# Kernel optimization log

Hardware: AMD Instinct MI355X
Metric: run time of the kernel (lower is better)

Reference implementation:

```python
import jax, jax.numpy as jnp
import numpy as np

D_MODEL = 256; N_HEADS = 8; D_FF = 1024; N_LAYERS = 8; N_BLOCKS = 4
VOCAB = 10000; N_SPARSE = 26; N_DENSE = 13; BATCH = 4096
SEQ = N_DENSE + N_SPARSE  # 39 feature tokens


def _ln(x, g, b, eps=1e-5):
    m = jnp.mean(x, -1, keepdims=True)
    v = jnp.mean((x - m) ** 2, -1, keepdims=True)
    return (x - m) * jax.lax.rsqrt(v + eps) * g + b


def _normalize(x, axis=-1, eps=1e-12):
    n = jnp.maximum(jnp.linalg.norm(x, axis=axis, keepdims=True), eps)
    return x / n


def setup_inputs() -> dict:
    key = jax.random.key(0)
    ks = iter(jax.random.split(key, 64))
    d, L, ff = D_MODEL, N_LAYERS, D_FF
    w = lambda shape: jax.random.normal(next(ks), shape, dtype=jnp.float32) * 0.02
    z = lambda shape: jnp.zeros(shape, jnp.float32)
    o = lambda shape: jnp.ones(shape, jnp.float32)
    return {
        "dense_x": jax.random.normal(next(ks), (BATCH, N_DENSE), dtype=jnp.float32),
        "sparse_x": jax.random.randint(next(ks), (BATCH, N_SPARSE), 0, VOCAB, dtype=jnp.int32),
        "W_dense": w((N_DENSE * d, N_DENSE)), "b_dense": z((N_DENSE * d,)),
        "emb": w((N_SPARSE, VOCAB + 1, d)),
        "Wq": w((L, d, d)), "bq": z((L, d)),
        "Wk": w((L, d, d)), "bk": z((L, d)),
        "Wv": w((L, d, d)), "bv": z((L, d)),
        "W1": w((L, ff, d)), "b1": z((L, ff)),
        "W2": w((L, d, ff)), "b2": z((L, d)),
        "n1g": o((L, d)), "n1b": z((L, d)),
        "n2g": o((L, d)), "n2b": z((L, d)),
        "qvec": w((N_BLOCKS, d)),
        "mha_in_w": w((3 * d, d)), "mha_in_b": z((3 * d,)),
        "mha_out_w": w((d, d)), "mha_out_b": z((d,)),
        "ng": o((d,)), "ngb": z((d,)),
        "Wo1": w((D_FF, SEQ * d)), "bo1": z((D_FF,)),
        "Wo2": w((1, D_FF)), "bo2": z((1,)),
    }


def reference(dense_x, sparse_x, W_dense, b_dense, emb, Wq, bq, Wk, bk, Wv, bv,
              W1, b1, W2, b2, n1g, n1b, n2g, n2b, qvec,
              mha_in_w, mha_in_b, mha_out_w, mha_out_b, ng, ngb,
              Wo1, bo1, Wo2, bo2):
    B = dense_x.shape[0]; d = D_MODEL; H = N_HEADS; dh = d // H
    # --- embed_features ---
    dense_emb = (dense_x @ W_dense.T + b_dense).reshape(B, N_DENSE, d)
    emb0 = emb.at[:, 0, :].set(0.0)  # padding_idx=0
    sp = emb0[jnp.arange(N_SPARSE), sparse_x]  # [B, 26, d]
    x = jnp.concatenate([dense_emb, sp], axis=1)  # [B, 39, d]

    scale = 1.0 / jnp.sqrt(jnp.float32(d))  # note: d_model, not head_dim
    block_size = N_LAYERS // N_BLOCKS
    block_outputs = [x]
    for i in range(N_LAYERS):
        # --- HSTU layer: sigmoid pointwise attention ---
        r = x
        h = _ln(x, n1g[i], n1b[i])
        q = (h @ Wq[i].T + bq[i]).reshape(B, SEQ, H, dh).transpose(0, 2, 1, 3)
        k = (h @ Wk[i].T + bk[i]).reshape(B, SEQ, H, dh).transpose(0, 2, 1, 3)
        v = (h @ Wv[i].T + bv[i]).reshape(B, SEQ, H, dh).transpose(0, 2, 1, 3)
        aw = jax.nn.sigmoid(jnp.einsum('bhqd,bhkd->bhqk', q, k) * scale)
        ao = jnp.einsum('bhqk,bhkd->bhqd', aw, v).transpose(0, 2, 1, 3).reshape(B, SEQ, d)
        x = r + ao
        r = x
        h = _ln(x, n2g[i], n2b[i])
        x = r + (jax.nn.relu(h @ W1[i].T + b1[i]) @ W2[i].T + b2[i])
        # --- AttentionResidual block mixing ---
        if (i + 1) % block_size == 0 and i < N_LAYERS - 1:
            V = jnp.stack(block_outputs + [x])  # [n, B, T, d]
            K = _normalize(V)
            qi = min(len(block_outputs), N_BLOCKS - 1)
            qn = _normalize(qvec[qi], axis=0)
            logits = jnp.einsum('d,nbtd->nbt', qn, K)
            wt = jax.nn.softmax(logits, axis=0)
            x = jnp.einsum('nbt,nbtd->btd', wt, V)
            block_outputs.append(x)

    # --- final LayerNorm + standard MHA residual ---
    r = x
    h = _ln(x, ng, ngb)
    qkv = h @ mha_in_w.T + mha_in_b
    q, k, v = jnp.split(qkv, 3, axis=-1)
    q = q.reshape(B, SEQ, H, dh).transpose(0, 2, 1, 3)
    k = k.reshape(B, SEQ, H, dh).transpose(0, 2, 1, 3)
    v = v.reshape(B, SEQ, H, dh).transpose(0, 2, 1, 3)
    at = jax.nn.softmax(jnp.einsum('bhqd,bhkd->bhqk', q, k) / jnp.sqrt(jnp.float32(dh)), axis=-1)
    mo = jnp.einsum('bhqk,bhkd->bhqd', at, v).transpose(0, 2, 1, 3).reshape(B, SEQ, d)
    x = r + (mo @ mha_out_w.T + mha_out_b)

    flat = x.reshape(B, -1)
    return (jax.nn.relu(flat @ Wo1.T + bo1) @ Wo2.T + bo2).squeeze(-1)
```

## Files before the change

kernel.cpp:

```cpp
#include <hip/hip_runtime.h>
#include <hip/hip_bf16.h>

typedef __attribute__((ext_vector_type(4))) float f32x4;
typedef __attribute__((ext_vector_type(8))) short short8;
typedef __attribute__((ext_vector_type(4))) unsigned short us4;

static __device__ __forceinline__ unsigned short f2bf(float f){
  return __builtin_bit_cast(unsigned short, __float2bfloat16(f));
}
static __device__ __forceinline__ float bf2f(unsigned short u){
  return __bfloat162float(__builtin_bit_cast(__hip_bfloat16, u));
}
static __device__ __forceinline__ short8 zero8(){
  short8 v;
#pragma unroll
  for (int e=0;e<8;++e) v[e]=0;
  return v;
}
static __device__ __forceinline__ void g2l16(const void* g, void* l){
  __builtin_amdgcn_global_load_lds(
    (const __attribute__((address_space(1))) unsigned int*)g,
    (__attribute__((address_space(3))) unsigned int*)l, 16, 0, 0);
}

template<int EPI>
__global__ __launch_bounds__(256)
void gemm_k(const unsigned short* __restrict__ Ap, int lda,
            const unsigned short* __restrict__ Bp,
            const float* __restrict__ bias,
            void* __restrict__ Outp, int ldo, int K,
            unsigned short* __restrict__ vT, int nColBlk)
{
  const int id = blockIdx.x;
  const int xcd = id & 7; const int t0 = id >> 3;
  const int cb = t0 % nColBlk; const int rb = (t0 / nColBlk)*8 + xcd;
  const long rowBase = (long)rb << 7;
  const long colBase = (long)cb << 7;
  const int tid = threadIdx.x, lane = tid & 63, w = tid >> 6;
  const int wm = (w >> 1) << 6, wn = (w & 1) << 6;
  const int cl = lane & 15, q4 = lane >> 4;

  __shared__ __align__(16) unsigned short As[128*64];
  __shared__ __align__(16) unsigned short Bs[128*64];

  const char* bSrc[4]; unsigned short* bDst[4];
  const char* aSrc[4]; unsigned short* aDst[4];
#pragma unroll
  for (int g=0; g<4; ++g){
    const int c = (w<<8) + (g<<6) + lane;
    const int r = c>>3, x = c&7, c16 = x ^ (r&7);
    bSrc[g] = (const char*)(Bp + (colBase + r)*(long)K) + c16*16;
    bDst[g] = Bs + (((w<<2)+g)<<9);
    aSrc[g] = (const char*)(Ap + (rowBase + r)*(long)lda) + c16*16;
    aDst[g] = As + (((w<<2)+g)<<9);
  }

  f32x4 acc[4][4];
#pragma unroll
  for (int m=0;m<4;++m)
#pragma unroll
    for (int n=0;n<4;++n) acc[m][n] = (f32x4){0.f,0.f,0.f,0.f};

  const int nk = K >> 6;
  for (int t=0; t<nk; ++t){
    if (t) __syncthreads();
    const long tb = (long)t << 7;
#pragma unroll
    for (int g=0; g<4; ++g){
      g2l16(bSrc[g] + tb, bDst[g]);
      g2l16(aSrc[g] + tb, aDst[g]);
    }
    __syncthreads();
#pragma unroll
    for (int ks=0; ks<2; ++ks){
      const int kb = ks*64 + (q4<<4);
      short8 af[4], bf_[4];
#pragma unroll
      for (int m=0;m<4;++m){
        const int r = wm + m*16 + cl;
        af[m] = *(const short8*)((const char*)As + r*128 + (kb ^ ((r&7)<<4)));
      }
#pragma unroll
      for (int n=0;n<4;++n){
        const int r = wn + n*16 + cl;
        bf_[n] = *(const short8*)((const char*)Bs + r*128 + (kb ^ ((r&7)<<4)));
      }
#pragma unroll
      for (int m=0;m<4;++m)
#pragma unroll
        for (int n=0;n<4;++n)
          acc[m][n] = __builtin_amdgcn_mfma_f32_16x16x32_bf16(af[m], bf_[n], acc[m][n], 0,0,0);
    }
  }

#pragma unroll
  for (int n=0;n<4;++n){
    const long col = colBase + wn + n*16 + cl;
    const float bi = bias[col];
#pragma unroll
    for (int m=0;m<4;++m){
      const long r0 = rowBase + wm + m*16 + (q4<<2);
#pragma unroll
      for (int i=0;i<4;++i){
        const float v = acc[m][n][i] + bi;
        const long row = r0 + i;
        if constexpr (EPI == 1){
          ((unsigned short*)Outp)[row*(long)ldo + col] = f2bf(fmaxf(v,0.f));
        } else {
          if (col < 512){
            ((unsigned short*)Outp)[row*512 + col] = f2bf(v);
          } else {
            const int bb = (int)row / 39;
            const int tt = (int)row - bb*39;
            unsigned short* vrow = vT + ((long)bb*256 + (col - 512))*48;
            vrow[tt] = f2bf(v);
            if (tt < 9) vrow[tt + 39] = 0;
          }
        }
      }
    }
  }
}

__global__ __launch_bounds__(512)
void ffn_k(const float* __restrict__ xf_in,
           const float* __restrict__ sB, const float* __restrict__ cB,
           const unsigned short* __restrict__ W1p,
           const float* __restrict__ b1p,
           const unsigned short* __restrict__ W2p,
           const float* __restrict__ b2p,
           float* __restrict__ xf,
           unsigned short* __restrict__ xln1)
{
  __shared__ __align__(16) unsigned short As[128*256];
  __shared__ __align__(16) unsigned short Wb1[64*256];
  __shared__ __align__(16) unsigned short Hs[128*64];
  __shared__ __align__(16) unsigned short Wb2[256*64];
  __shared__ float part1[512], part2[512];
  __shared__ float sln[128], cln[128];

  const int tid = threadIdx.x, lane = tid & 63, w = tid >> 6;
  const int cl = lane & 15, q4 = lane >> 4;
  const long rowBase = (long)blockIdx.x << 7;
  const int wm = (w >> 2) << 6, wn = (w & 3) << 6;

  {
    const int r = tid >> 2, kq = tid & 3;
    const float s = sB[rowBase + r], c = cB[rowBase + r];
    const float* src = xf_in + (rowBase + r)*256 + (kq<<6);
    unsigned short* tile = As + (kq<<13);
#pragma unroll
    for (int g=0; g<8; ++g){
      f32x4 a = *(const f32x4*)(src + g*8);
      f32x4 b = *(const f32x4*)(src + g*8 + 4);
      short8 v;
#pragma unroll
      for (int e=0;e<4;++e){ v[e] = (short)f2bf(a[e]*s + c); v[4+e] = (short)f2bf(b[e]*s + c); }
      *(short8*)((char*)tile + r*128 + ((g*16) ^ ((r&7)<<4))) = v;
    }
  }

  f32x4 acc[4][4];
#pragma unroll
  for (int m=0;m<4;++m)
#pragma unroll
    for (int n=0;n<4;++n) acc[m][n] = (f32x4){0.f,0.f,0.f,0.f};

  for (int j=0; j<16; ++j){
    const int ffbase = j<<6;
    __syncthreads();
#pragma unroll
    for (int it=0; it<4; ++it){
      const int g = tid + (it<<9);
      {
        const int kt = g>>9, cc = g&511, rr = cc>>3, xs = cc&7;
        g2l16(W1p + ((long)(ffbase+rr))*256 + (kt<<6) + ((xs^(rr&7))<<3),
              Wb1 + (((tid & ~63) + (it<<9))<<3));
      }
      {
        const int rr = g>>3, xs = g&7;
        g2l16(W2p + (long)rr*1024 + ffbase + ((xs^(rr&7))<<3),
              Wb2 + (((tid & ~63) + (it<<9))<<3));
      }
    }
    float b1v[4];
#pragma unroll
    for (int n=0;n<4;++n) b1v[n] = b1p[ffbase + n*16 + cl];
    __syncthreads();

    f32x4 hacc[4];
#pragma unroll
    for (int n=0;n<4;++n) hacc[n] = (f32x4){0.f,0.f,0.f,0.f};
    const int ar = (w<<4) + cl;
#pragma unroll
    for (int kt=0; kt<4; ++kt)
#pragma unroll
      for (int ks=0; ks<2; ++ks){
        const int kb = ks*64 + (q4<<4);
        short8 af = *(const short8*)((const char*)As + (kt<<14) + ar*128 + (kb ^ ((ar&7)<<4)));
#pragma unroll
        for (int n=0;n<4;++n){
          const int rn = n*16 + cl;
          short8 bf_ = *(const short8*)((const char*)Wb1 + (kt<<13) + rn*128 + (kb ^ ((rn&7)<<4)));
          hacc[n] = __builtin_amdgcn_mfma_f32_16x16x32_bf16(af, bf_, hacc[n], 0,0,0);
        }
      }
#pragma unroll
    for (int n=0;n<4;++n)
#pragma unroll
      for (int i=0;i<4;++i){
        const int hr = (w<<4) + (q4<<2) + i, hc = n*16 + cl;
        const float hv = fmaxf(hacc[n][i] + b1v[n], 0.f);
        *(unsigned short*)((char*)Hs + hr*128 + ((hc*2) ^ ((hr&7)<<4))) = f2bf(hv);
      }
    __syncthreads();

#pragma unroll
    for (int ks=0; ks<2; ++ks){
      const int kb = ks*64 + (q4<<4);
      short8 am[4], bm[4];
#pragma unroll
      for (int m=0;m<4;++m){
        const int r = wm + m*16 + cl;
        am[m] = *(const short8*)((const char*)Hs + r*128 + (kb ^ ((r&7)<<4)));
      }
#pragma unroll
      for (int n=0;n<4;++n){
        const int r = wn + n*16 + cl;
        bm[n] = *(const short8*)((const char*)Wb2 + r*128 + (kb ^ ((r&7)<<4)));
      }
#pragma unroll
      for (int m=0;m<4;++m)
#pragma unroll
        for (int n=0;n<4;++n)
          acc[m][n] = __builtin_amdgcn_mfma_f32_16x16x32_bf16(am[m], bm[n], acc[m][n], 0,0,0);
    }
  }

#pragma unroll
  for (int n=0;n<4;++n){
    const int col = wn + n*16 + cl;
    const float bi = b2p[col];
#pragma unroll
    for (int m=0;m<4;++m)
#pragma unroll
      for (int i=0;i<4;++i){
        const int row = wm + m*16 + (q4<<2) + i;
        const long gi = (rowBase + row)*256 + col;
        const float v = acc[m][n][i] + bi + xf[gi];
        acc[m][n][i] = v;
        xf[gi] = v;
      }
  }
#pragma unroll
  for (int m=0;m<4;++m)
#pragma unroll
    for (int i=0;i<4;++i){
      float s1 = 0.f, s2 = 0.f;
#pragma unroll
      for (int n=0;n<4;++n){ const float v = acc[m][n][i]; s1 += v; s2 += v*v; }
#pragma unroll
      for (int off=8; off; off>>=1){ s1 += __shfl_xor(s1, off, 16); s2 += __shfl_xor(s2, off, 16); }
      const int row = wm + m*16 + (q4<<2) + i;
      if (cl == 0){ part1[row*4 + (w&3)] = s1; part2[row*4 + (w&3)] = s2; }
    }
  __syncthreads();
  if (tid < 128){
    const float S1 = part1[tid*4]+part1[tid*4+1]+part1[tid*4+2]+part1[tid*4+3];
    const float S2 = part2[tid*4]+part2[tid*4+1]+part2[tid*4+2]+part2[tid*4+3];
    const float mn = S1*(1.f/256.f);
    const float var = S2*(1.f/256.f) - mn*mn;
    const float s = rsqrtf(var + 1e-5f);
    sln[tid] = s; cln[tid] = -mn*s;
  }
  __syncthreads();
#pragma unroll
  for (int m=0;m<4;++m)
#pragma unroll
    for (int i=0;i<4;++i){
      const int row = wm + m*16 + (q4<<2) + i;
      const float s = sln[row], c = cln[row];
#pragma unroll
      for (int n=0;n<4;++n){
        const int col = wn + n*16 + cl;
        xln1[(rowBase + row)*256 + col] = f2bf(acc[m][n][i]*s + c);
      }
    }
}

__global__ __launch_bounds__(256)
void attn_sig_k(const unsigned short* __restrict__ qkb,
                const unsigned short* __restrict__ vT,
                float* xf, float* __restrict__ sB, float* __restrict__ cB)
{
  __shared__ __align__(16) unsigned short Ps[4*48*64];
  __shared__ float part[312];

  const int b = blockIdx.x;
  const int tid = threadIdx.x, lane = tid & 63, w = tid >> 6;
  const int cl = lane & 15, q4 = lane >> 4;
  unsigned short* P = Ps + w*3072;
  const unsigned short* qb = qkb + (long)b*39*512;
  const unsigned short* vbb = vT + (long)b*256*48;

  if (lane < 48){
    const int r = lane;
    *(short8*)((char*)P + r*128 + (96  ^ ((r&7)<<4))) = zero8();
    *(short8*)((char*)P + r*128 + (112 ^ ((r&7)<<4))) = zero8();
  }

  float ps1[3][4], ps2[3][4];
#pragma unroll
  for (int m=0;m<3;++m)
#pragma unroll
    for (int i=0;i<4;++i){ ps1[m][i]=0.f; ps2[m][i]=0.f; }

#pragma unroll
  for (int hh=0; hh<2; ++hh){
    const int h = (w<<1) + hh;
    f32x4 sac[3][3];
#pragma unroll
    for (int m=0;m<3;++m)
#pragma unroll
      for (int n=0;n<3;++n) sac[m][n] = (f32x4){0.f,0.f,0.f,0.f};
    short8 aq[3], bk8[3];
#pragma unroll
    for (int m=0;m<3;++m){
      const int r = m*16 + cl;
      aq[m] = (r < 39) ? *(const short8*)(qb + (long)r*512 + h*32 + q4*8) : zero8();
    }
#pragma unroll
    for (int n=0;n<3;++n){
      const int r = n*16 + cl;
      bk8[n] = (r < 39) ? *(const short8*)(qb + (long)r*512 + 256 + h*32 + q4*8) : zero8();
    }
#pragma unroll
    for (int m=0;m<3;++m)
#pragma unroll
      for (int n=0;n<3;++n)
        sac[m][n] = __builtin_amdgcn_mfma_f32_16x16x32_bf16(aq[m], bk8[n], sac[m][n], 0,0,0);
#pragma unroll
    for (int m=0;m<3;++m)
#pragma unroll
      for (int n=0;n<3;++n)
#pragma unroll
        for (int i=0;i<4;++i){
          const int row = m*16 + (q4<<2) + i, col = n*16 + cl;
          const float pv = 1.f/(1.f + __expf(-sac[m][n][i]*0.0625f));
          *(unsigned short*)((char*)P + row*128 + ((col*2) ^ ((row&7)<<4))) = f2bf(pv);
        }
    f32x4 aoc[3][2];
#pragma unroll
    for (int m=0;m<3;++m)
#pragma unroll
      for (int n=0;n<2;++n) aoc[m][n] = (f32x4){0.f,0.f,0.f,0.f};
#pragma unroll
    for (int ks=0; ks<2; ++ks){
      const int kb = ks*64 + (q4<<4);
      short8 pa[3], vb[2];
#pragma unroll
      for (int m=0;m<3;++m){
        const int r = m*16 + cl;
        pa[m] = *(const short8*)((const char*)P + r*128 + (kb ^ ((r&7)<<4)));
      }
#pragma unroll
      for (int n=0;n<2;++n){
        vb[n] = zero8();
        if (ks == 0 || q4 < 2)
          vb[n] = *(const short8*)(vbb + (long)(h*32 + n*16 + cl)*48 + ks*32 + q4*8);
      }
#pragma unroll
      for (int m=0;m<3;++m)
#pragma unroll
        for (int n=0;n<2;++n)
          aoc[m][n] = __builtin_amdgcn_mfma_f32_16x16x32_bf16(pa[m], vb[n], aoc[m][n], 0,0,0);
    }
#pragma unroll
    for (int m=0;m<3;++m)
#pragma unroll
      for (int n=0;n<2;++n)
#pragma unroll
        for (int i=0;i<4;++i){
          const int row = m*16 + (q4<<2) + i;
          if (row < 39){
            const long gi = (((long)(b*39+row))<<8) + h*32 + n*16 + cl;
            const float nv = xf[gi] + aoc[m][n][i];
            xf[gi] = nv;
            ps1[m][i] += nv; ps2[m][i] += nv*nv;
          }
        }
  }
#pragma unroll
  for (int m=0;m<3;++m)
#pragma unroll
    for (int i=0;i<4;++i){
      float a1 = ps1[m][i], a2 = ps2[m][i];
#pragma unroll
      for (int off=8; off; off>>=1){ a1 += __shfl_xor(a1, off, 16); a2 += __shfl_xor(a2, off, 16); }
      const int row = m*16 + (q4<<2) + i;
      if (cl == 0 && row < 39){ part[row*8 + (w<<1)] = a1; part[row*8 + (w<<1) + 1] = a2; }
    }
  __syncthreads();
  if (tid < 39){
    const float S1 = part[tid*8]+part[tid*8+2]+part[tid*8+4]+part[tid*8+6];
    const float S2 = part[tid*8+1]+part[tid*8+3]+part[tid*8+5]+part[tid*8+7];
    const float mn = S1*(1.f/256.f);
    const float var = S2*(1.f/256.f) - mn*mn;
    const float s = rsqrtf(var + 1e-5f);
    sB[b*39+tid] = s; cB[b*39+tid] = -mn*s;
  }
}

__global__ __launch_bounds__(256)
void attn_fin_k(const unsigned short* __restrict__ qkb,
                const unsigned short* __restrict__ vT,
                const float* __restrict__ xf,
                const unsigned short* __restrict__ moW,
                const float* __restrict__ moB,
                unsigned short* __restrict__ flatb)
{
  __shared__ __align__(16) unsigned short Ps[4*48*64];
  __shared__ __align__(16) unsigned short Mo[48*256];

  const int b = blockIdx.x;
  const int tid = threadIdx.x, lane = tid & 63, w = tid >> 6;
  const int cl = lane & 15, q4 = lane >> 4;
  unsigned short* P = Ps + w*3072;
  const unsigned short* qb = qkb + (long)b*39*512;
  const unsigned short* vbb = vT + (long)b*256*48;
  const float SC = 0.17677669529663687f;

  if (lane < 48){
    const int r = lane;
    *(short8*)((char*)P + r*128 + (96  ^ ((r&7)<<4))) = zero8();
    *(short8*)((char*)P + r*128 + (112 ^ ((r&7)<<4))) = zero8();
  }

#pragma unroll
  for (int hh=0; hh<2; ++hh){
    const int h = (w<<1) + hh;
    f32x4 sac[3][3];
#pragma unroll
    for (int m=0;m<3;++m)
#pragma unroll
      for (int n=0;n<3;++n) sac[m][n] = (f32x4){0.f,0.f,0.f,0.f};
    short8 aq[3], bk8[3];
#pragma unroll
    for (int m=0;m<3;++m){
      const int r = m*16 + cl;
      aq[m] = (r < 39) ? *(const short8*)(qb + (long)r*512 + h*32 + q4*8) : zero8();
    }
#pragma unroll
    for (int n=0;n<3;++n){
      const int r = n*16 + cl;
      bk8[n] = (r < 39) ? *(const short8*)(qb + (long)r*512 + 256 + h*32 + q4*8) : zero8();
    }
#pragma unroll
    for (int m=0;m<3;++m)
#pragma unroll
      for (int n=0;n<3;++n)
        sac[m][n] = __builtin_amdgcn_mfma_f32_16x16x32_bf16(aq[m], bk8[n], sac[m][n], 0,0,0);
#pragma unroll
    for (int m=0;m<3;++m)
#pragma unroll
      for (int i=0;i<4;++i){
        const float v0 = sac[m][0][i]*SC, v1 = sac[m][1][i]*SC, v2 = sac[m][2][i]*SC;
        const bool c2ok = (32 + cl) < 39;
        float mx = fmaxf(v0, v1);
        if (c2ok) mx = fmaxf(mx, v2);
#pragma unroll
        for (int off=8; off; off>>=1) mx = fmaxf(mx, __shfl_xor(mx, off, 16));
        const float e0 = __expf(v0-mx), e1 = __expf(v1-mx);
        const float e2 = c2ok ? __expf(v2-mx) : 0.f;
        float s = e0+e1+e2;
#pragma unroll
        for (int off=8; off; off>>=1) s += __shfl_xor(s, off, 16);
        const float inv = 1.f/s;
        const int row = m*16 + (q4<<2) + i;
        *(unsigned short*)((char*)P + row*128 + (((cl   )*2) ^ ((row&7)<<4))) = f2bf(e0*inv);
        *(unsigned short*)((char*)P + row*128 + (((16+cl)*2) ^ ((row&7)<<4))) = f2bf(e1*inv);
        *(unsigned short*)((char*)P + row*128 + (((32+cl)*2) ^ ((row&7)<<4))) = f2bf(e2*inv);
      }
    f32x4 aoc[3][2];
#pragma unroll
    for (int m=0;m<3;++m)
#pragma unroll
      for (int n=0;n<2;++n) aoc[m][n] = (f32x4){0.f,0.f,0.f,0.f};
#pragma unroll
    for (int ks=0; ks<2; ++ks){
      const int kb = ks*64 + (q4<<4);
      short8 pa[3], vb[2];
#pragma unroll
      for (int m=0;m<3;++m){
        const int r = m*16 + cl;
        pa[m] = *(const short8*)((const char*)P + r*128 + (kb ^ ((r&7)<<4)));
      }
#pragma unroll
      for (int n=0;n<2;++n){
        vb[n] = zero8();
        if (ks == 0 || q4 < 2)
          vb[n] = *(const short8*)(vbb + (long)(h*32 + n*16 + cl)*48 + ks*32 + q4*8);
      }
#pragma unroll
      for (int m=0;m<3;++m)
#pragma unroll
        for (int n=0;n<2;++n)
          aoc[m][n] = __builtin_amdgcn_mfma_f32_16x16x32_bf16(pa[m], vb[n], aoc[m][n], 0,0,0);
    }
#pragma unroll
    for (int m=0;m<3;++m)
#pragma unroll
      for (int n=0;n<2;++n)
#pragma unroll
        for (int i=0;i<4;++i){
          const int row = m*16 + (q4<<2) + i;
          const int colq = h*32 + n*16 + cl;
          *(unsigned short*)((char*)Mo + row*512 + ((colq*2) ^ ((row&7)<<4))) = f2bf(aoc[m][n][i]);
        }
  }
  __syncthreads();
  f32x4 oc[3][4];
#pragma unroll
  for (int m=0;m<3;++m)
#pragma unroll
    for (int n=0;n<4;++n) oc[m][n] = (f32x4){0.f,0.f,0.f,0.f};
#pragma unroll
  for (int ks=0; ks<8; ++ks){
    const int kb = ks*64 + (q4<<4);
    short8 am[3], bm[4];
#pragma unroll
    for (int m=0;m<3;++m){
      const int r = m*16 + cl;
      am[m] = *(const short8*)((const char*)Mo + r*512 + (kb ^ ((r&7)<<4)));
    }
#pragma unroll
    for (int n=0;n<4;++n){
      const int nn = (w<<6) + n*16 + cl;
      bm[n] = *(const short8*)(moW + (long)nn*256 + ks*32 + q4*8);
    }
#pragma unroll
    for (int m=0;m<3;++m)
#pragma unroll
      for (int n=0;n<4;++n)
        oc[m][n] = __builtin_amdgcn_mfma_f32_16x16x32_bf16(am[m], bm[n], oc[m][n], 0,0,0);
  }
#pragma unroll
  for (int m=0;m<3;++m)
#pragma unroll
    for (int n=0;n<4;++n)
#pragma unroll
      for (int i=0;i<4;++i){
        const int row = m*16 + (q4<<2) + i;
        if (row < 39){
          const int col = (w<<6) + n*16 + cl;
          const float v = oc[m][n][i] + moB[col] + xf[(((long)(b*39+row))<<8) + col];
          flatb[(long)b*9984 + row*256 + col] = f2bf(v);
        }
      }
}

__global__ __launch_bounds__(256)
void embed_k(const float* __restrict__ dense_x, const int* __restrict__ sparse_x,
             const float* __restrict__ W_dense, const float* __restrict__ b_dense,
             const float* __restrict__ emb,
             float* __restrict__ xf, unsigned short* __restrict__ x0b,
             unsigned short* __restrict__ xln1)
{
  const int bid = blockIdx.x;
  const int b = bid / 39, t = bid - b*39;
  const int c = threadIdx.x;
  float v;
  if (t < 13){
    const int j = t*256 + c;
    v = b_dense[j];
    const float* wr = W_dense + (long)j*13;
    const float* dx = dense_x + (long)b*13;
#pragma unroll
    for (int k2=0;k2<13;++k2) v = fmaf(dx[k2], wr[k2], v);
  } else {
    const int idx = sparse_x[b*26 + (t-13)];
    v = (idx == 0) ? 0.f : emb[((long)(t-13)*10001 + idx)*256 + c];
  }
  const long row = bid;
  xf[row*256 + c] = v;
  x0b[row*256 + c] = f2bf(v);
  float s1 = v, s2 = v*v;
#pragma unroll
  for (int off=32; off; off>>=1){ s1 += __shfl_xor(s1, off); s2 += __shfl_xor(s2, off); }
  __shared__ float r1[4], r2[4];
  const int lane = c & 63, wq = c >> 6;
  if (lane == 0){ r1[wq]=s1; r2[wq]=s2; }
  __syncthreads();
  const float S1 = r1[0]+r1[1]+r1[2]+r1[3];
  const float S2 = r2[0]+r2[1]+r2[2]+r2[3];
  const float mn = S1*(1.f/256.f);
  const float var = S2*(1.f/256.f) - mn*mn;
  const float s = rsqrtf(var+1e-5f);
  xln1[row*256 + c] = f2bf((v - mn)*s);
}

template<int NSRC>
__global__ __launch_bounds__(256)
void mix_k(float* __restrict__ xf,
           const unsigned short* __restrict__ s0,
           const unsigned short* __restrict__ s1p,
           const unsigned short* __restrict__ s2p,
           unsigned short* mout,
           const float* __restrict__ qvec, int qi,
           unsigned short* __restrict__ xln1)
{
  const int b = blockIdx.x;
  const int tid = threadIdx.x, lane = tid&63, w = tid>>6;
  const int c4 = lane << 2;
  f32x4 q = *(const f32x4*)(qvec + qi*256 + c4);
  float qq = q[0]*q[0]+q[1]*q[1]+q[2]*q[2]+q[3]*q[3];
#pragma unroll
  for (int off=32; off; off>>=1) qq += __shfl_xor(qq, off);
  const float qsc = 1.f/fmaxf(sqrtf(qq), 1e-12f);
#pragma unroll
  for (int e=0;e<4;++e) q[e] *= qsc;
  for (int t = w; t < 39; t += 4){
    const long ro = ((long)(b*39+t))*256 + c4;
    f32x4 v[NSRC];
#pragma unroll
    for (int n=0;n<NSRC;++n){
      if (n == NSRC-1) v[n] = *(const f32x4*)(xf + ro);
      else {
        const unsigned short* sp = (n==0)?s0:((n==1)?s1p:s2p);
        us4 u = *(const us4*)(sp + ro);
#pragma unroll
        for (int e=0;e<4;++e) v[n][e] = bf2f(u[e]);
      }
    }
    float lg[NSRC];
#pragma unroll
    for (int n=0;n<NSRC;++n){
      float nn = v[n][0]*v[n][0]+v[n][1]*v[n][1]+v[n][2]*v[n][2]+v[n][3]*v[n][3];
      float dd = q[0]*v[n][0]+q[1]*v[n][1]+q[2]*v[n][2]+q[3]*v[n][3];
#pragma unroll
      for (int off=32; off; off>>=1){ nn += __shfl_xor(nn,off); dd += __shfl_xor(dd,off); }
      lg[n] = dd / fmaxf(sqrtf(nn), 1e-12f);
    }
    float mx = lg[0];
#pragma unroll
    for (int n=1;n<NSRC;++n) mx = fmaxf(mx, lg[n]);
    float es = 0.f, e_[NSRC];
#pragma unroll
    for (int n=0;n<NSRC;++n){ e_[n] = __expf(lg[n]-mx); es += e_[n]; }
    const float inv = 1.f/es;
    f32x4 o = {0.f,0.f,0.f,0.f};
#pragma unroll
    for (int n=0;n<NSRC;++n){
      const float wt = e_[n]*inv;
#pragma unroll
      for (int e=0;e<4;++e) o[e] = fmaf(wt, v[n][e], o[e]);
    }
    *(f32x4*)(xf + ro) = o;
    if (mout){
      us4 u;
#pragma unroll
      for (int e=0;e<4;++e) u[e] = f2bf(o[e]);
      *(us4*)(mout + ro) = u;
    }
    float s1 = o[0]+o[1]+o[2]+o[3];
    float s2 = o[0]*o[0]+o[1]*o[1]+o[2]*o[2]+o[3]*o[3];
#pragma unroll
    for (int off=32; off; off>>=1){ s1 += __shfl_xor(s1,off); s2 += __shfl_xor(s2,off); }
    const float mn = s1*(1.f/256.f);
    const float var = s2*(1.f/256.f)-mn*mn;
    const float s = rsqrtf(var+1e-5f);
    const float c = -mn*s;
    us4 u2;
#pragma unroll
    for (int e=0;e<4;++e) u2[e] = f2bf(o[e]*s + c);
    *(us4*)(xln1 + ro) = u2;
  }
}

__global__ __launch_bounds__(256)
void head2_k(const unsigned short* __restrict__ h1h, const float* __restrict__ Wo2,
             const float* __restrict__ bo2, float* __restrict__ outp)
{
  const int b = blockIdx.x*4 + (threadIdx.x>>6);
  const int lane = threadIdx.x & 63;
  float s = 0.f;
#pragma unroll
  for (int g=0; g<2; ++g){
    const int base = lane*16 + g*8;
    short8 v8 = *(const short8*)(h1h + (long)b*1024 + base);
#pragma unroll
    for (int e=0;e<8;++e) s = fmaf(bf2f((unsigned short)v8[e]), Wo2[base+e], s);
  }
#pragma unroll
  for (int off=32; off; off>>=1) s += __shfl_xor(s, off);
  if (lane==0) outp[b] = s + bo2[0];
}

__global__ void cvt_k(const float* __restrict__ src, unsigned short* __restrict__ dst, long n){
  const long i = (long)blockIdx.x*256 + threadIdx.x;
  if (i < n) dst[i] = f2bf(src[i]);
}
__global__ void prep_qkv_k(const float* Wq, const float* Wk, const float* Wv,
                           const float* g, unsigned short* dst){
  const int n = blockIdx.x, i = blockIdx.y, k = threadIdx.x;
  const int sel = n >> 8, nn = n & 255;
  const float* W = sel==0?Wq:(sel==1?Wk:Wv);
  dst[((long)i*768 + n)*256 + k] = f2bf(W[((long)i*256+nn)*256 + k] * g[i*256+k]);
}
__global__ void prep_qkvb_k(const float* Wq,const float* Wk,const float* Wv,
                            const float* bq,const float* bk,const float* bv,
                            const float* beta, float* dst){
  const int n = blockIdx.x, i = blockIdx.y, k = threadIdx.x;
  const int sel = n>>8, nn = n&255;
  const float* W = sel==0?Wq:(sel==1?Wk:Wv);
  const float* bb = sel==0?bq:(sel==1?bk:bv);
  float v = beta[i*256+k] * W[((long)i*256+nn)*256+k];
  __shared__ float r[4];
#pragma unroll
  for (int off=32; off; off>>=1) v += __shfl_xor(v, off);
  if ((k&63)==0) r[k>>6] = v;
  __syncthreads();
  if (k==0) dst[i*768+n] = bb[i*256+nn] + r[0]+r[1]+r[2]+r[3];
}
__global__ void prep_w1_k(const float* W1, const float* g, unsigned short* dst){
  const int n = blockIdx.x, i = blockIdx.y, k = threadIdx.x;
  const long o = ((long)i*1024+n)*256 + k;
  dst[o] = f2bf(W1[o] * g[i*256+k]);
}
__global__ void prep_w1b_k(const float* W1, const float* b1, const float* beta, float* dst){
  const int n = blockIdx.x, i = blockIdx.y, k = threadIdx.x;
  float v = beta[i*256+k] * W1[((long)i*1024+n)*256+k];
  __shared__ float r[4];
#pragma unroll
  for (int off=32; off; off>>=1) v += __shfl_xor(v, off);
  if ((k&63)==0) r[k>>6] = v;
  __syncthreads();
  if (k==0) dst[i*1024+n] = b1[i*1024+n] + r[0]+r[1]+r[2]+r[3];
}
__global__ void prep_mha_k(const float* W, const float* g, unsigned short* dst){
  const int n = blockIdx.x, k = threadIdx.x;
  dst[n*256+k] = f2bf(W[n*256+k]*g[k]);
}
__global__ void prep_mhab_k(const float* W, const float* bb, const float* beta, float* dst){
  const int n = blockIdx.x, k = threadIdx.x;
  float v = beta[k]*W[n*256+k];
  __shared__ float r[4];
#pragma unroll
  for (int off=32; off; off>>=1) v += __shfl_xor(v, off);
  if ((k&63)==0) r[k>>6] = v;
  __syncthreads();
  if (k==0) dst[n] = bb[n] + r[0]+r[1]+r[2]+r[3];
}

extern "C" void kernel_launch(void* const* d_in, const int* in_sizes, int n_in,
                              void* d_out, int out_size, void* d_ws, size_t ws_size,
                              hipStream_t stream)
{
  (void)in_sizes; (void)n_in; (void)out_size; (void)ws_size;
  const float* dense_x  = (const float*)d_in[0];
  const int*   sparse_x = (const int*)d_in[1];
  const float* W_dense  = (const float*)d_in[2];
  const float* b_dense  = (const float*)d_in[3];
  const float* emb      = (const float*)d_in[4];
  const float* Wq = (const float*)d_in[5];
  const float* bq = (const float*)d_in[6];
  const float* Wk = (const float*)d_in[7];
  const float* bk = (const float*)d_in[8];
  const float* Wv = (const float*)d_in[9];
  const float* bv = (const float*)d_in[10];
  const float* W1 = (const float*)d_in[11];
  const float* b1 = (const float*)d_in[12];
  const float* W2 = (const float*)d_in[13];
  const float* b2 = (const float*)d_in[14];
  const float* n1g= (const float*)d_in[15];
  const float* n1b= (const float*)d_in[16];
  const float* n2g= (const float*)d_in[17];
  const float* n2b= (const float*)d_in[18];
  const float* qvec=(const float*)d_in[19];
  const float* mha_in_w = (const float*)d_in[20];
  const float* mha_in_b = (const float*)d_in[21];
  const float* mha_out_w= (const float*)d_in[22];
  const float* mha_out_b= (const float*)d_in[23];
  const float* ng = (const float*)d_in[24];
  const float* ngb= (const float*)d_in[25];
  const float* Wo1= (const float*)d_in[26];
  const float* bo1= (const float*)d_in[27];
  const float* Wo2= (const float*)d_in[28];
  const float* bo2= (const float*)d_in[29];

  char* ws = (char*)d_ws;
  size_t off = 0;
  auto alloc = [&](size_t bytes)->void*{ void* p = ws + off; off += (bytes + 255) & ~(size_t)255; return p; };
  float* xf            = (float*)alloc(163577856ull);
  unsigned short* qkh  = (unsigned short*)alloc(163577856ull);
  unsigned short* vT   = (unsigned short*)alloc(100663296ull);
  unsigned short* x0b  = (unsigned short*)alloc(81788928ull);
  unsigned short* m1b  = (unsigned short*)alloc(81788928ull);
  unsigned short* m2b  = (unsigned short*)alloc(81788928ull);
  unsigned short* xln1 = (unsigned short*)alloc(81788928ull);
  unsigned short* h1h  = (unsigned short*)alloc(8388608ull);
  float* sB = (float*)alloc(638976ull);
  float* cB = (float*)alloc(638976ull);
  unsigned short* Wqkv_f = (unsigned short*)alloc(3145728ull);
  float* bqkv_f = (float*)alloc(24576ull);
  unsigned short* W1_f = (unsigned short*)alloc(4194304ull);
  float* b1_f = (float*)alloc(32768ull);
  unsigned short* W2_f = (unsigned short*)alloc(4194304ull);
  unsigned short* mhain_f = (unsigned short*)alloc(393216ull);
  float* mhainb_f = (float*)alloc(3072ull);
  unsigned short* mhaout_f = (unsigned short*)alloc(131072ull);
  unsigned short* Wo1_f = (unsigned short*)alloc(20447232ull);

  unsigned short* flatb = m1b;

  cvt_k<<<8192,256,0,stream>>>(W2, W2_f, 2097152L);
  cvt_k<<<256,256,0,stream>>>(mha_out_w, mhaout_f, 65536L);
  cvt_k<<<39936,256,0,stream>>>(Wo1, Wo1_f, 10223616L);
  prep_qkv_k<<<dim3(768,8),256,0,stream>>>(Wq,Wk,Wv,n1g,Wqkv_f);
  prep_qkvb_k<<<dim3(768,8),256,0,stream>>>(Wq,Wk,Wv,bq,bk,bv,n1b,bqkv_f);
  prep_w1_k<<<dim3(1024,8),256,0,stream>>>(W1,n2g,W1_f);
  prep_w1b_k<<<dim3(1024,8),256,0,stream>>>(W1,b1,n2b,b1_f);
  prep_mha_k<<<768,256,0,stream>>>(mha_in_w, ng, mhain_f);
  prep_mhab_k<<<768,256,0,stream>>>(mha_in_w, mha_in_b, ngb, mhainb_f);

  embed_k<<<159744,256,0,stream>>>(dense_x, sparse_x, W_dense, b_dense, emb, xf, x0b, xln1);

  for (int i = 0; i < 8; ++i){
    gemm_k<3><<<7488,256,0,stream>>>(xln1, 256,
        Wqkv_f + (size_t)i*196608, bqkv_f + i*768, qkh, 512, 256, vT, 6);
    attn_sig_k<<<4096,256,0,stream>>>(qkh, vT, xf, sB, cB);
    ffn_k<<<1248,512,0,stream>>>(xf, sB, cB,
        W1_f + (size_t)i*262144, b1_f + i*1024,
        W2_f + (size_t)i*262144, b2 + i*256, xf, xln1);
    if (i == 1)      mix_k<2><<<4096,256,0,stream>>>(xf, x0b, m1b, m2b, m1b, qvec, 1, xln1);
    else if (i == 3) mix_k<3><<<4096,256,0,stream>>>(xf, x0b, m1b, m2b, m2b, qvec, 2, xln1);
    else if (i == 5) mix_k<4><<<4096,256,0,stream>>>(xf, x0b, m1b, m2b, nullptr, qvec, 3, xln1);
  }
  gemm_k<3><<<7488,256,0,stream>>>(xln1, 256, mhain_f, mhainb_f, qkh, 512, 256, vT, 6);
  attn_fin_k<<<4096,256,0,stream>>>(qkh, vT, xf, mhaout_f, mha_out_b, flatb);
  gemm_k<1><<<256,256,0,stream>>>(flatb, 9984, Wo1_f, bo1, h1h, 1024, 9984, nullptr, 8);
  head2_k<<<1024,256,0,stream>>>(h1h, Wo2, bo2, (float*)d_out);
}
```

Measured before the change: 6.970 ms.

## Keep FFN input activations in registers and alias reduction scratch into weight LDS

Each wave's 16-row slice of the normalized input is now loaded straight from global memory into eight bf16 registers, instead of being staged in a 64KB shared-memory A tile. The small LayerNorm reduction buffers reuse the W1 staging buffer, with an extra barrier added before they are written. Launch bounds now request 4 waves per SIMD. Together these cut LDS use per block from roughly 140KB to about 64KB, which should let more blocks share a CU. The cost is higher VGPR pressure from holding the A fragments and the tighter launch bound, which could cause spills.

New measurement: 8.973 ms. 28.7% more time.

```diff
diff --git a/kernel.cpp b/kernel.cpp
--- a/kernel.cpp
+++ b/kernel.cpp
@@ -122,7 +122,7 @@
   }
 }
 
-__global__ __launch_bounds__(512)
+__global__ __launch_bounds__(512, 4)
 void ffn_k(const float* __restrict__ xf_in,
            const float* __restrict__ sB, const float* __restrict__ cB,
            const unsigned short* __restrict__ W1p,
@@ -132,31 +132,32 @@
            float* __restrict__ xf,
            unsigned short* __restrict__ xln1)
 {
-  __shared__ __align__(16) unsigned short As[128*256];
   __shared__ __align__(16) unsigned short Wb1[64*256];
+  __shared__ __align__(16) unsigned short Wb2[256*64];
   __shared__ __align__(16) unsigned short Hs[128*64];
-  __shared__ __align__(16) unsigned short Wb2[256*64];
-  __shared__ float part1[512], part2[512];
-  __shared__ float sln[128], cln[128];
+  float* part1 = (float*)Wb1;
+  float* part2 = part1 + 512;
+  float* sln   = part2 + 512;
+  float* cln   = sln + 128;
 
   const int tid = threadIdx.x, lane = tid & 63, w = tid >> 6;
   const int cl = lane & 15, q4 = lane >> 4;
   const long rowBase = (long)blockIdx.x << 7;
   const int wm = (w >> 2) << 6, wn = (w & 3) << 6;
 
+  short8 af[8];
   {
-    const int r = tid >> 2, kq = tid & 3;
-    const float s = sB[rowBase + r], c = cB[rowBase + r];
-    const float* src = xf_in + (rowBase + r)*256 + (kq<<6);
-    unsigned short* tile = As + (kq<<13);
-#pragma unroll
-    for (int g=0; g<8; ++g){
-      f32x4 a = *(const f32x4*)(src + g*8);
-      f32x4 b = *(const f32x4*)(src + g*8 + 4);
+    const int row = (w<<4) + cl;
+    const float s = sB[rowBase + row], c = cB[rowBase + row];
+    const float* src = xf_in + (rowBase + row)*256 + (q4<<3);
+#pragma unroll
+    for (int kt=0; kt<8; ++kt){
+      f32x4 a = *(const f32x4*)(src + kt*32);
+      f32x4 b = *(const f32x4*)(src + kt*32 + 4);
       short8 v;
 #pragma unroll
       for (int e=0;e<4;++e){ v[e] = (short)f2bf(a[e]*s + c); v[4+e] = (short)f2bf(b[e]*s + c); }
-      *(short8*)((char*)tile + r*128 + ((g*16) ^ ((r&7)<<4))) = v;
+      af[kt] = v;
     }
   }
 
@@ -191,18 +192,17 @@
     f32x4 hacc[4];
 #pragma unroll
     for (int n=0;n<4;++n) hacc[n] = (f32x4){0.f,0.f,0.f,0.f};
-    const int ar = (w<<4) + cl;
-#pragma unroll
-    for (int kt=0; kt<4; ++kt)
+#pragma unroll
+    for (int kt2=0; kt2<4; ++kt2)
 #pragma unroll
       for (int ks=0; ks<2; ++ks){
         const int kb = ks*64 + (q4<<4);
-        short8 af = *(const short8*)((const char*)As + (kt<<14) + ar*128 + (kb ^ ((ar&7)<<4)));
+        const short8 a = af[kt2*2 + ks];
 #pragma unroll
         for (int n=0;n<4;++n){
           const int rn = n*16 + cl;
-          short8 bf_ = *(const short8*)((const char*)Wb1 + (kt<<13) + rn*128 + (kb ^ ((rn&7)<<4)));
-          hacc[n] = __builtin_amdgcn_mfma_f32_16x16x32_bf16(af, bf_, hacc[n], 0,0,0);
+          short8 bf_ = *(const short8*)((const char*)Wb1 + (kt2<<13) + rn*128 + (kb ^ ((rn&7)<<4)));
+          hacc[n] = __builtin_amdgcn_mfma_f32_16x16x32_bf16(a, bf_, hacc[n], 0,0,0);
         }
       }
 #pragma unroll
@@ -252,6 +252,7 @@
         xf[gi] = v;
       }
   }
+  __syncthreads();
 #pragma unroll
   for (int m=0;m<4;++m)
 #pragma unroll
```

## Read FFN weight fragments directly from global memory instead of staging in LDS

Applied to the files above, without the earlier changes.

The FFN kernel no longer copies W1 and W2 tiles into shared memory each iteration. MFMA B-operands are loaded straight from global memory, relying on L2 and cache reuse across blocks, and the LayerNorm scratch arrays now alias the As buffer. This removes two weight LDS buffers and the sync before each tile, cutting LDS use so more blocks can be resident (launch bounds set to 4). The cost is higher global and L2 traffic with more latency exposed on weight loads, since every wave redundantly loads its own fragments.

Result: slower. 11.44 ms (+64.1%).

```diff
diff --git a/kernel.cpp b/kernel.cpp
--- a/kernel.cpp
+++ b/kernel.cpp
@@ -122,7 +122,7 @@
   }
 }
 
-__global__ __launch_bounds__(512)
+__global__ __launch_bounds__(512, 4)
 void ffn_k(const float* __restrict__ xf_in,
            const float* __restrict__ sB, const float* __restrict__ cB,
            const unsigned short* __restrict__ W1p,
@@ -133,11 +133,11 @@
            unsigned short* __restrict__ xln1)
 {
   __shared__ __align__(16) unsigned short As[128*256];
-  __shared__ __align__(16) unsigned short Wb1[64*256];
   __shared__ __align__(16) unsigned short Hs[128*64];
-  __shared__ __align__(16) unsigned short Wb2[256*64];
-  __shared__ float part1[512], part2[512];
-  __shared__ float sln[128], cln[128];
+  float* part1 = (float*)As;
+  float* part2 = part1 + 512;
+  float* sln   = part2 + 512;
+  float* cln   = sln + 128;
 
   const int tid = threadIdx.x, lane = tid & 63, w = tid >> 6;
   const int cl = lane & 15, q4 = lane >> 4;
@@ -159,6 +159,7 @@
       *(short8*)((char*)tile + r*128 + ((g*16) ^ ((r&7)<<4))) = v;
     }
   }
+  __syncthreads();
 
   f32x4 acc[4][4];
 #pragma unroll
@@ -168,26 +169,9 @@
 
   for (int j=0; j<16; ++j){
     const int ffbase = j<<6;
-    __syncthreads();
-#pragma unroll
-    for (int it=0; it<4; ++it){
-      const int g = tid + (it<<9);
-      {
-        const int kt = g>>9, cc = g&511, rr = cc>>3, xs = cc&7;
-        g2l16(W1p + ((long)(ffbase+rr))*256 + (kt<<6) + ((xs^(rr&7))<<3),
-              Wb1 + (((tid & ~63) + (it<<9))<<3));
-      }
-      {
-        const int rr = g>>3, xs = g&7;
-        g2l16(W2p + (long)rr*1024 + ffbase + ((xs^(rr&7))<<3),
-              Wb2 + (((tid & ~63) + (it<<9))<<3));
-      }
-    }
     float b1v[4];
 #pragma unroll
     for (int n=0;n<4;++n) b1v[n] = b1p[ffbase + n*16 + cl];
-    __syncthreads();
-
     f32x4 hacc[4];
 #pragma unroll
     for (int n=0;n<4;++n) hacc[n] = (f32x4){0.f,0.f,0.f,0.f};
@@ -197,12 +181,12 @@
 #pragma unroll
       for (int ks=0; ks<2; ++ks){
         const int kb = ks*64 + (q4<<4);
-        short8 af = *(const short8*)((const char*)As + (kt<<14) + ar*128 + (kb ^ ((ar&7)<<4)));
+        const short8 a = *(const short8*)((const char*)As + (kt<<14) + ar*128 + (kb ^ ((ar&7)<<4)));
 #pragma unroll
         for (int n=0;n<4;++n){
-          const int rn = n*16 + cl;
-          short8 bf_ = *(const short8*)((const char*)Wb1 + (kt<<13) + rn*128 + (kb ^ ((rn&7)<<4)));
-          hacc[n] = __builtin_amdgcn_mfma_f32_16x16x32_bf16(af, bf_, hacc[n], 0,0,0);
+          const long rn = ffbase + n*16 + cl;
+          const short8 bf_ = *(const short8*)(W1p + rn*256 + (kt<<6) + ks*32 + (q4<<3));
+          hacc[n] = __builtin_amdgcn_mfma_f32_16x16x32_bf16(a, bf_, hacc[n], 0,0,0);
         }
       }
 #pragma unroll
@@ -226,8 +210,8 @@
       }
 #pragma unroll
       for (int n=0;n<4;++n){
-        const int r = wn + n*16 + cl;
-        bm[n] = *(const short8*)((const char*)Wb2 + r*128 + (kb ^ ((r&7)<<4)));
+        const long rr = wn + n*16 + cl;
+        bm[n] = *(const short8*)(W2p + rr*1024 + ffbase + ks*32 + (q4<<3));
       }
 #pragma unroll
       for (int m=0;m<4;++m)
@@ -235,6 +219,7 @@
         for (int n=0;n<4;++n)
           acc[m][n] = __builtin_amdgcn_mfma_f32_16x16x32_bf16(am[m], bm[n], acc[m][n], 0,0,0);
     }
+    __syncthreads();
   }
 
 #pragma unroll
@@ -252,6 +237,7 @@
         xf[gi] = v;
       }
   }
+  __syncthreads();
 #pragma unroll
   for (int m=0;m<4;++m)
 #pragma unroll
```
